# Kernel optimization log

Measured on AMD Instinct MI355X. Metric: run time of the kernel, lower is better.

Reference implementation:

```python
import jax, jax.numpy as jnp
import numpy as np
from jax import lax

N = 2048
D_ENC = 64      # conv channels
D = 512         # node embedding dim (resnet18 feature dim)
K = 5           # max_num_neighbors
L_LAYERS = 4    # num_layers
ARENA = 32.0    # positions scaled to [0, ARENA)^2
R2 = 2.0        # radius^2 = (sqrt(2))^2


def setup_inputs() -> dict:
    key = jax.random.key(0)
    ks = jax.random.split(key, 9)
    imgs = jax.random.normal(ks[0], (N, 3, 64, 64), dtype=jnp.float32)
    pos = jax.random.uniform(ks[1], (N, 2), dtype=jnp.float32)  # scaled by ARENA inside
    conv_w = jax.random.normal(ks[2], (D_ENC, 3, 7, 7), dtype=jnp.float32) * 0.05
    conv_b = jnp.zeros((D_ENC,), dtype=jnp.float32)
    proj_w = jax.random.normal(ks[3], (D_ENC, D), dtype=jnp.float32) * (1.0 / np.sqrt(D_ENC))
    proj_b = jnp.zeros((D,), dtype=jnp.float32)
    w_self = jax.random.normal(ks[4], (L_LAYERS, D, D), dtype=jnp.float32) * (1.0 / np.sqrt(D))
    w_nbr = jax.random.normal(ks[5], (L_LAYERS, D, D), dtype=jnp.float32) * (1.0 / np.sqrt(D))
    b_gnn = jnp.zeros((L_LAYERS, D), dtype=jnp.float32)
    return {"imgs": imgs, "pos": pos, "conv_w": conv_w, "conv_b": conv_b,
            "proj_w": proj_w, "proj_b": proj_b,
            "w_self": w_self, "w_nbr": w_nbr, "b_gnn": b_gnn}


def _encode(imgs, conv_w, conv_b, proj_w, proj_b):
    # conv 7x7 stride 2 + relu + global avg pool + linear -> [N, D]
    x = lax.conv_general_dilated(imgs, conv_w, window_strides=(2, 2), padding="SAME",
                                 dimension_numbers=("NCHW", "OIHW", "NCHW"))
    x = jax.nn.relu(x + conv_b[None, :, None, None])
    x = x.mean(axis=(2, 3))                      # [N, D_ENC]
    return jax.nn.relu(x @ proj_w + proj_b)      # [N, D]


def _radius_knn(pos):
    # radius graph with radius sqrt(2), no self loops, capped at K neighbors
    p = pos * ARENA                              # [N, 2]
    d2 = jnp.sum((p[:, None, :] - p[None, :, :]) ** 2, axis=-1)  # [N, N]
    invalid = (d2 > R2) | jnp.eye(N, dtype=bool)
    d2m = jnp.where(invalid, jnp.inf, d2)
    neg_vals, idx = lax.top_k(-d2m, K)           # K nearest within radius
    valid = jnp.isfinite(neg_vals)               # [N, K]
    return idx, valid


def reference(imgs, pos, conv_w, conv_b, proj_w, proj_b, w_self, w_nbr, b_gnn):
    h = _encode(imgs, conv_w, conv_b, proj_w, proj_b)   # [N, D]
    idx, valid = _radius_knn(pos)                        # [N, K], [N, K]
    vmask = valid.astype(h.dtype)                        # [N, K]
    denom = jnp.maximum(vmask.sum(axis=1, keepdims=True), 1.0)  # [N, 1]
    for l in range(L_LAYERS):
        nbr = h[idx] * vmask[:, :, None]                 # [N, K, D] gather
        agg = nbr.sum(axis=1) / denom                    # mean over valid neighbors
        h = jax.nn.relu(h @ w_self[l] + agg @ w_nbr[l] + b_gnn[l])
    return h
```

## Files before the change

### kernel.cpp

```cpp
#include <hip/hip_runtime.h>


#define NNODES 2048

typedef __attribute__((ext_vector_type(8))) _Float16 half8;
typedef __attribute__((ext_vector_type(16))) float f32x16;

__device__ inline uint pack2h(float x, float y) {
  ushort a = __builtin_bit_cast(ushort, (_Float16)x);
  ushort b = __builtin_bit_cast(ushort, (_Float16)y);
  return (uint)a | ((uint)b << 16);
}

__global__ __launch_bounds__(256) void setup_kernel(
    const float* __restrict__ conv_w, const float* __restrict__ wsrc_s,
    const float* __restrict__ wsrc_n, const float* __restrict__ pos,
    ushort* __restrict__ wfrag, ushort* __restrict__ wT,
    int* __restrict__ nbr, float* __restrict__ den, float* __restrict__ enc) {
  __shared__ float4 smem4[1040];
  const int bid = blockIdx.x;
  const int tid = threadIdx.x;

  if (bid < 44) {
    int i = bid * 256 + tid;
    int j = i & 7;
    int l = (i >> 3) & 63;
    int q = i >> 9;
    int kb = q % 11, ct = q / 11;
    int g = 2 * kb + (l >> 5);
    int c = 32 * ct + (l & 31);
    float val = 0.f;
    if (g < 21 && j < 7) val = conv_w[c * 147 + g * 7 + j];
    wfrag[i] = __builtin_bit_cast(ushort, (_Float16)val);
    return;
  }

  if (bid < 556) {
    float(*s)[65] = (float(*)[65])smem4;
    int bid2 = bid - 44;
    int m = bid2 >> 6, kt = (bid2 >> 3) & 7, nt = bid2 & 7;
    const float* in = (m < 4) ? (wsrc_s + m * 262144) : (wsrc_n + (m - 4) * 262144);
    ushort* out = wT + m * 262144;
    int k0 = kt << 6, n0 = nt << 6;
#pragma unroll
    for (int rep = 0; rep < 4; ++rep) {
      int row = (rep << 4) + (tid >> 4);
      int c4 = (tid & 15) << 2;
      float4 v = *(const float4*)&in[(k0 + row) * 512 + n0 + c4];
      s[row][c4] = v.x; s[row][c4 + 1] = v.y; s[row][c4 + 2] = v.z; s[row][c4 + 3] = v.w;
    }
    __syncthreads();
#pragma unroll
    for (int rep = 0; rep < 4; ++rep) {
      int n = (rep << 4) + (tid >> 4);
      int k4 = (tid & 15) << 2;
      ushort4 o;
      o.x = __builtin_bit_cast(ushort, (_Float16)s[k4 + 0][n]);
      o.y = __builtin_bit_cast(ushort, (_Float16)s[k4 + 1][n]);
      o.z = __builtin_bit_cast(ushort, (_Float16)s[k4 + 2][n]);
      o.w = __builtin_bit_cast(ushort, (_Float16)s[k4 + 3][n]);
      *(ushort4*)&out[(n0 + n) * 512 + k0 + k4] = o;
    }
    return;
  }

  {
    float* s_d2 = (float*)smem4;
    int* s_idx = (int*)(s_d2 + NNODES);
    int* s_cnt = (int*)(s_idx + NNODES);
    const int i = bid - 556;
    if (tid < 16) {
      float4 z4 = {0.f, 0.f, 0.f, 0.f};
      ((float4*)(enc + i * 64))[tid] = z4;
    }
    if (tid == 0) *s_cnt = 0;
    __syncthreads();
    const float px = pos[2 * i] * 32.f, py = pos[2 * i + 1] * 32.f;
#pragma unroll
    for (int r = 0; r < 8; ++r) {
      int j = tid + (r << 8);
      float2 q = ((const float2*)pos)[j];
      float dx = q.x * 32.f - px, dy = q.y * 32.f - py;
      float d2 = dx * dx + dy * dy;
      if (d2 <= 2.0f && j != i) {
        int slot = atomicAdd(s_cnt, 1);
        s_d2[slot] = d2;
        s_idx[slot] = j;
      }
    }
    __syncthreads();
    if (tid < 64) {
      const int lane = tid;
      const int cnt = *s_cnt;
      int nf = 0;
#pragma unroll
      for (int k = 0; k < 5; ++k) {
        float best = 1e30f;
        int bslot = 0x7fffffff;
        for (int e = lane; e < cnt; e += 64) {
          float d = s_d2[e];
          if (d < best) { best = d; bslot = e; }
        }
#pragma unroll
        for (int off = 1; off < 64; off <<= 1) {
          float od = __shfl_xor(best, off);
          int os = __shfl_xor(bslot, off);
          if (od < best || (od == best && os < bslot)) { best = od; bslot = os; }
        }
        bool got = (best < 1e30f);
        if (lane == 0) nbr[i * 5 + k] = got ? s_idx[bslot] : -1;
        if (got) { s_d2[bslot] = 1e30f; ++nf; }
      }
      if (lane == 0) den[i] = 1.f / (float)(nf > 0 ? nf : 1);
    }
  }
}

__global__ __launch_bounds__(256) void conv_pool_kernel(
    const float* __restrict__ imgs, const ushort* __restrict__ wfrag,
    const float* __restrict__ cb, float* __restrict__ enc) {
  __shared__ int4 s_all[2471];
  ushort* s_img = (ushort*)s_all;
  const half8* swf8 = (const half8*)((char*)s_all + 15984);
  float* s_pool = (float*)((char*)s_all + 38512);

  const int n = blockIdx.x >> 1;
  const int r0half = blockIdx.x & 1;
  const int wy = 32 * r0half - 2;
  const int tid = threadIdx.x;
  const int lane = tid & 63;
  const int w = tid >> 6;
  const int hi = lane >> 5;
  const int lo = lane & 31;

  int4 z = {0, 0, 0, 0};
  for (int i = tid; i < 999; i += 256) s_all[i] = z;
  __syncthreads();

  {
    const int4* wf4 = (const int4*)wfrag;
    int4* swf4 = (int4*)((char*)s_all + 15984);
    for (int i = tid; i < 1408; i += 256) swf4[i] = wf4[i];
  }

  const float4* src = (const float4*)(imgs + (size_t)n * 12288);
  for (int i = tid; i < 1776; i += 256) {
    int ic = i / 592;
    int rem = i - ic * 592;
    int li = rem >> 4, xq = rem & 15;
    int iy = wy + li;
    if (iy >= 0 && iy < 64) {
      float4 v = src[(ic * 64 + iy) * 16 + xq];
      int d = (ic * 37 + li) * 72 + (xq << 2) + 2;
      ((uint*)s_img)[d >> 1] = pack2h(v.x, v.y);
      ((uint*)s_img)[(d >> 1) + 1] = pack2h(v.z, v.w);
    }
  }

  int aoff[11];
#pragma unroll
  for (int kb = 0; kb < 11; ++kb) {
    int g = 2 * kb + hi;
    if (g > 20) g = 20;
    int ic = g / 7, ky = g - ic * 7;
    aoff[kb] = (ic * 37 + ky) * 144 + 4 * lo + w * 1152;
  }
  const float bias0 = cb[lo];
  const float bias1 = cb[32 + lo];
  __syncthreads();

  const char* sb = (const char*)s_img;
  union F { half8 v; uint u[4]; };
  F A0, A1, A2, A3, C0, C1, C2, C3;
  half8 B0, B1, D0, D1;
  f32x16 acc00 = {}, acc01 = {}, acc10 = {}, acc11 = {};
  f32x16 acc20 = {}, acc21 = {}, acc30 = {}, acc31 = {};

#define LOADSET(AA0, AA1, AA2, AA3, BB0, BB1, KB) do {                        \
    const char* p_ = (const char*)__builtin_assume_aligned(sb + aoff[KB], 4); \
    __builtin_memcpy(&AA0.u[0], p_,        8);                                \
    __builtin_memcpy(&AA0.u[2], p_ + 8,    8);                                \
    __builtin_memcpy(&AA1.u[0], p_ + 288,  8);                                \
    __builtin_memcpy(&AA1.u[2], p_ + 296,  8);                                \
    __builtin_memcpy(&AA2.u[0], p_ + 576,  8);                                \
    __builtin_memcpy(&AA2.u[2], p_ + 584,  8);                                \
    __builtin_memcpy(&AA3.u[0], p_ + 864,  8);                                \
    __builtin_memcpy(&AA3.u[2], p_ + 872,  8);                                \
    BB0 = swf8[(KB) * 64 + lane];                                             \
    BB1 = swf8[(11 + (KB)) * 64 + lane];                                      \
  } while (0)

#define MFMA8(AA0, AA1, AA2, AA3, BB0, BB1) do {                              \
    __builtin_amdgcn_s_setprio(1);                                            \
    acc00 = __builtin_amdgcn_mfma_f32_32x32x16_f16(AA0.v, BB0, acc00, 0, 0, 0); \
    acc01 = __builtin_amdgcn_mfma_f32_32x32x16_f16(AA0.v, BB1, acc01, 0, 0, 0); \
    acc10 = __builtin_amdgcn_mfma_f32_32x32x16_f16(AA1.v, BB0, acc10, 0, 0, 0); \
    acc11 = __builtin_amdgcn_mfma_f32_32x32x16_f16(AA1.v, BB1, acc11, 0, 0, 0); \
    acc20 = __builtin_amdgcn_mfma_f32_32x32x16_f16(AA2.v, BB0, acc20, 0, 0, 0); \
    acc21 = __builtin_amdgcn_mfma_f32_32x32x16_f16(AA2.v, BB1, acc21, 0, 0, 0); \
    acc30 = __builtin_amdgcn_mfma_f32_32x32x16_f16(AA3.v, BB0, acc30, 0, 0, 0); \
    acc31 = __builtin_amdgcn_mfma_f32_32x32x16_f16(AA3.v, BB1, acc31, 0, 0, 0); \
    __builtin_amdgcn_s_setprio(0);                                            \
  } while (0)

  LOADSET(A0, A1, A2, A3, B0, B1, 0);
#pragma unroll
  for (int kb = 0; kb < 10; kb += 2) {
    LOADSET(C0, C1, C2, C3, D0, D1, kb + 1);
    MFMA8(A0, A1, A2, A3, B0, B1);
    LOADSET(A0, A1, A2, A3, B0, B1, kb + 2);
    MFMA8(C0, C1, C2, C3, D0, D1);
  }
  MFMA8(A0, A1, A2, A3, B0, B1);
#undef LOADSET
#undef MFMA8

  float s0 = 0.f, s1 = 0.f;
#pragma unroll
  for (int r = 0; r < 16; ++r) {
    s0 += fmaxf(acc00[r] + bias0, 0.f) + fmaxf(acc10[r] + bias0, 0.f)
        + fmaxf(acc20[r] + bias0, 0.f) + fmaxf(acc30[r] + bias0, 0.f);
    s1 += fmaxf(acc01[r] + bias1, 0.f) + fmaxf(acc11[r] + bias1, 0.f)
        + fmaxf(acc21[r] + bias1, 0.f) + fmaxf(acc31[r] + bias1, 0.f);
  }
  s0 += __shfl_xor(s0, 32);
  s1 += __shfl_xor(s1, 32);
  if (lane < 32) {
    s_pool[w * 64 + lo] = s0;
    s_pool[w * 64 + 32 + lo] = s1;
  }
  __syncthreads();
  if (tid < 64) {
    float s = s_pool[tid] + s_pool[64 + tid] + s_pool[128 + tid] + s_pool[192 + tid];
    atomicAdd(&enc[n * 64 + tid], s * (1.f / 1024.f));
  }
}

__global__ __launch_bounds__(256) void proj_kernel(
    const float* __restrict__ enc, const float* __restrict__ pw,
    const float* __restrict__ pb, ushort* __restrict__ h16) {
  int c = ((blockIdx.x & 1) << 8) | threadIdx.x;
  int r0 = (blockIdx.x >> 1) << 3;
  float bias = pb[c];
  float acc[8];
#pragma unroll
  for (int r = 0; r < 8; ++r) acc[r] = bias;
#pragma unroll 4
  for (int k = 0; k < 64; ++k) {
    float w = pw[k * 512 + c];
#pragma unroll
    for (int r = 0; r < 8; ++r) acc[r] = fmaf(enc[(r0 + r) * 64 + k], w, acc[r]);
  }
#pragma unroll
  for (int r = 0; r < 8; ++r)
    h16[(r0 + r) * 512 + c] = __builtin_bit_cast(ushort, (_Float16)fmaxf(acc[r], 0.f));
}

__global__ __launch_bounds__(256) void gnn_gemm_kernel(
    const ushort* __restrict__ h16, const int* __restrict__ nbr,
    const float* __restrict__ den,
    const ushort* __restrict__ Ws, const ushort* __restrict__ Wn,
    const float* __restrict__ bias, ushort* __restrict__ hout,
    float* __restrict__ fout, int final_layer) {
  __shared__ ushort s_lds[2][16384];
  __shared__ int s_nbr[320];
  __shared__ float s_den[64];
  const int tid = threadIdx.x;
  const int lane = tid & 63;
  const int hi = lane >> 5, lo = lane & 31;
  const int wu = __builtin_amdgcn_readfirstlane(tid >> 6);
  const int wr = wu >> 1, wc = wu & 1;
  const int bm = blockIdx.x >> 3, bn = blockIdx.x & 7;
  const int r0 = bm << 6, c0 = bn << 6;

  if (tid < 80) ((int4*)s_nbr)[tid] = ((const int4*)(nbr + r0 * 5))[tid];
  else if (tid < 96) ((float4*)s_den)[tid - 80] = ((const float4*)(den + r0))[tid - 80];
  __syncthreads();

  const int grow = tid >> 2, gseg = tid & 3;
  int gj[5];
  uint gm[5];
#pragma unroll
  for (int k = 0; k < 5; ++k) {
    int j = s_nbr[grow * 5 + k];
    gm[k] = (j >= 0) ? 0xFFFFFFFFu : 0u;
    gj[k] = (j >= 0) ? j : 0;
  }
  half8 den8;
  {
    _Float16 dh = (_Float16)s_den[grow];
#pragma unroll
    for (int e = 0; e < 8; ++e) den8[e] = dh;
  }

  union GU { half8 v; uint u[4]; };
  GU ga[5][2];

  auto GATHER = [&](int it) {
    const ushort* hb = h16 + (it << 6) + gseg * 16;
#pragma unroll
    for (int k = 0; k < 5; ++k) {
      const half8* p = (const half8*)(hb + gj[k] * 512);
      ga[k][0].v = p[0];
      ga[k][1].v = p[1];
    }
  };
  auto COMBINE = [&](int buf) {
#pragma unroll
    for (int part = 0; part < 2; ++part) {
      GU t0, t1, t2, t3, t4;
#pragma unroll
      for (int j2 = 0; j2 < 4; ++j2) {
        t0.u[j2] = ga[0][part].u[j2] & gm[0];
        t1.u[j2] = ga[1][part].u[j2] & gm[1];
        t2.u[j2] = ga[2][part].u[j2] & gm[2];
        t3.u[j2] = ga[3][part].u[j2] & gm[3];
        t4.u[j2] = ga[4][part].u[j2] & gm[4];
      }
      half8 s = ((t0.v + t1.v) + (t2.v + t3.v)) + t4.v;
      s = s * den8;
      *(half8*)&s_lds[buf][4096 + (2 * gseg + part) * 512 + grow * 8] = s;
    }
  };
  auto STAGE = [&](int buf, int it) {
    int k0 = it << 6;
    const ushort* ph = h16 + (r0 + lane) * 512 + k0 + 8 * wu;
    const ushort* ps = Ws + (c0 + lane) * 512 + k0 + 8 * wu;
    const ushort* pn = Wn + (c0 + lane) * 512 + k0 + 8 * wu;
    ushort* lb = &s_lds[buf][wu << 9];
#define GLDS(SRC, DST) __builtin_amdgcn_global_load_lds( \
      (const __attribute__((address_space(1))) void*)(SRC), \
      (__attribute__((address_space(3))) void*)(DST), 16, 0, 0)
    GLDS(ph, lb);            GLDS(ph + 32, lb + 2048);
    GLDS(ps, lb + 8192);     GLDS(ps + 32, lb + 10240);
    GLDS(pn, lb + 12288);    GLDS(pn + 32, lb + 14336);
#undef GLDS
  };

  f32x16 accS = {}, accN = {};
  GATHER(0);
  STAGE(0, 0);
  COMBINE(0);
  __syncthreads();
  int cur = 0;
  for (int it = 0; it < 8; ++it) {
    if (it < 7) {
      GATHER(it + 1);
      STAGE(cur ^ 1, it + 1);
    }
    const half8* pAh = (const half8*)&s_lds[cur][0];
    const half8* pAg = (const half8*)&s_lds[cur][4096];
    const half8* pBs = (const half8*)&s_lds[cur][8192];
    const half8* pBn = (const half8*)&s_lds[cur][12288];
#pragma unroll
    for (int ks = 0; ks < 4; ++ks) {
      int gi = (2 * ks + hi) * 64;
      half8 ah = pAh[gi + 32 * wr + lo];
      half8 bs = pBs[gi + 32 * wc + lo];
      accS = __builtin_amdgcn_mfma_f32_32x32x16_f16(ah, bs, accS, 0, 0, 0);
      half8 ag = pAg[gi + 32 * wr + lo];
      half8 bn2 = pBn[gi + 32 * wc + lo];
      accN = __builtin_amdgcn_mfma_f32_32x32x16_f16(ag, bn2, accN, 0, 0, 0);
    }
    if (it < 7) COMBINE(cur ^ 1);
    __syncthreads();
    cur ^= 1;
  }

  const int col = c0 + 32 * wc + lo;
  const float b = bias[col];
#pragma unroll
  for (int r = 0; r < 16; ++r) {
    int row = r0 + 32 * wr + (r & 3) + ((r >> 2) << 3) + (hi << 2);
    float v = fmaxf(accS[r] + accN[r] + b, 0.f);
    if (final_layer) fout[row * 512 + col] = v;
    else hout[row * 512 + col] = __builtin_bit_cast(ushort, (_Float16)v);
  }
}

extern "C" void kernel_launch(void* const* d_in, const int* in_sizes, int n_in,
                              void* d_out, int out_size, void* d_ws, size_t ws_size,
                              hipStream_t stream) {
  const float* imgs   = (const float*)d_in[0];
  const float* pos    = (const float*)d_in[1];
  const float* conv_w = (const float*)d_in[2];
  const float* conv_b = (const float*)d_in[3];
  const float* proj_w = (const float*)d_in[4];
  const float* proj_b = (const float*)d_in[5];
  const float* w_self = (const float*)d_in[6];
  const float* w_nbr  = (const float*)d_in[7];
  const float* b_gnn  = (const float*)d_in[8];

  char* ws = (char*)d_ws;
  ushort* wfrag = (ushort*)(ws);
  float*  enc   = (float*) (ws + 32768);
  ushort* h16a  = (ushort*)(ws + 557056);
  ushort* h16b  = (ushort*)(ws + 2654208);
  ushort* wT16  = (ushort*)(ws + 6848512);
  int*    nbr   = (int*)   (ws + 11042816);
  float*  den   = (float*) (ws + 11083776);

  setup_kernel<<<2604, 256, 0, stream>>>(conv_w, w_self, w_nbr, pos,
                                         wfrag, wT16, nbr, den, enc);
  conv_pool_kernel<<<2 * NNODES, 256, 0, stream>>>(imgs, wfrag, conv_b, enc);
  proj_kernel<<<512, 256, 0, stream>>>(enc, proj_w, proj_b, h16a);

  for (int l = 0; l < 4; ++l) {
    ushort* hin  = (l & 1) ? h16b : h16a;
    ushort* hnew = (l & 1) ? h16a : h16b;
    gnn_gemm_kernel<<<256, 256, 0, stream>>>(
        hin, nbr, den, wT16 + l * 262144, wT16 + (4 + l) * 262144,
        b_gnn + l * 512, hnew, (float*)d_out, (l == 3) ? 1 : 0);
  }
}
```

Baseline: 158.3 us.

## Split conv MFMA into two row passes, async-load weights to LDS, raise occupancy

Restructures the conv MFMA loop to process the four row tiles in two passes of two, halving the live accumulator registers, and sets launch bounds to request four blocks per CU. Weight fragments are now copied to LDS with global_load_lds direct-to-LDS instructions issued before the first barrier, overlapping with the LDS zeroing and avoiding the register round-trip. A-operand addressing uses precomputed bases with constant offsets instead of an offset array. The trade-off is that B fragments are reloaded from LDS in each pass, and the larger unrolled code may add instruction overhead.

```diff
diff --git a/kernel.cpp b/kernel.cpp
--- a/kernel.cpp
+++ b/kernel.cpp
@@ -116,12 +116,11 @@
   }
 }
 
-__global__ __launch_bounds__(256) void conv_pool_kernel(
+__global__ __launch_bounds__(256, 4) void conv_pool_kernel(
     const float* __restrict__ imgs, const ushort* __restrict__ wfrag,
     const float* __restrict__ cb, float* __restrict__ enc) {
   __shared__ int4 s_all[2471];
   ushort* s_img = (ushort*)s_all;
-  const half8* swf8 = (const half8*)((char*)s_all + 15984);
   float* s_pool = (float*)((char*)s_all + 38512);
 
   const int n = blockIdx.x >> 1;
@@ -135,13 +134,22 @@
 
   int4 z = {0, 0, 0, 0};
   for (int i = tid; i < 999; i += 256) s_all[i] = z;
+
+  {
+    char* ldsb = (char*)s_all + 15984;
+#pragma unroll
+    for (int r = 0; r < 5; ++r) {
+      __builtin_amdgcn_global_load_lds(
+          (const __attribute__((address_space(1))) void*)(wfrag + (r * 256 + tid) * 8),
+          (__attribute__((address_space(3))) void*)(ldsb + (r * 256 + tid) * 16), 16, 0, 0);
+    }
+    if (tid < 128) {
+      __builtin_amdgcn_global_load_lds(
+          (const __attribute__((address_space(1))) void*)(wfrag + (1280 + tid) * 8),
+          (__attribute__((address_space(3))) void*)(ldsb + (1280 + tid) * 16), 16, 0, 0);
+    }
+  }
   __syncthreads();
-
-  {
-    const int4* wf4 = (const int4*)wfrag;
-    int4* swf4 = (int4*)((char*)s_all + 15984);
-    for (int i = tid; i < 1408; i += 256) swf4[i] = wf4[i];
-  }
 
   const float4* src = (const float4*)(imgs + (size_t)n * 12288);
   for (int i = tid; i < 1776; i += 256) {
@@ -157,77 +165,84 @@
     }
   }
 
-  int aoff[11];
-#pragma unroll
-  for (int kb = 0; kb < 11; ++kb) {
-    int g = 2 * kb + hi;
-    if (g > 20) g = 20;
-    int ic = g / 7, ky = g - ic * 7;
-    aoff[kb] = (ic * 37 + ky) * 144 + 4 * lo + w * 1152;
-  }
   const float bias0 = cb[lo];
   const float bias1 = cb[32 + lo];
   __syncthreads();
 
   const char* sb = (const char*)s_img;
+  const char* baseA = sb + 4 * lo + w * 1152 + (hi ? 144 : 0);
+  const char* baseA3 = sb + 4 * lo + w * 1152 + (hi ? 5328 : 864);
+  const char* baseB = (const char*)s_all + 15984 + lane * 16;
+
+
   union F { half8 v; uint u[4]; };
-  F A0, A1, A2, A3, C0, C1, C2, C3;
-  half8 B0, B1, D0, D1;
-  f32x16 acc00 = {}, acc01 = {}, acc10 = {}, acc11 = {};
-  f32x16 acc20 = {}, acc21 = {}, acc30 = {}, acc31 = {};
-
-#define LOADSET(AA0, AA1, AA2, AA3, BB0, BB1, KB) do {                        \
-    const char* p_ = (const char*)__builtin_assume_aligned(sb + aoff[KB], 4); \
-    __builtin_memcpy(&AA0.u[0], p_,        8);                                \
-    __builtin_memcpy(&AA0.u[2], p_ + 8,    8);                                \
-    __builtin_memcpy(&AA1.u[0], p_ + 288,  8);                                \
-    __builtin_memcpy(&AA1.u[2], p_ + 296,  8);                                \
-    __builtin_memcpy(&AA2.u[0], p_ + 576,  8);                                \
-    __builtin_memcpy(&AA2.u[2], p_ + 584,  8);                                \
-    __builtin_memcpy(&AA3.u[0], p_ + 864,  8);                                \
-    __builtin_memcpy(&AA3.u[2], p_ + 872,  8);                                \
-    BB0 = swf8[(KB) * 64 + lane];                                             \
-    BB1 = swf8[(11 + (KB)) * 64 + lane];                                      \
+  float poolacc0 = 0.f, poolacc1 = 0.f;
+
+#define LOADA(F0, F1, BASE, OFF, TP) do {                                     \
+    const uint* p_ = (const uint*)((BASE) + (OFF) + (TP) * 576);              \
+    F0.u[0] = p_[0]; F0.u[1] = p_[1]; F0.u[2] = p_[2]; F0.u[3] = p_[3];       \
+    const uint* q_ = (const uint*)((BASE) + (OFF) + (TP) * 576 + 288);        \
+    F1.u[0] = q_[0]; F1.u[1] = q_[1]; F1.u[2] = q_[2]; F1.u[3] = q_[3];       \
   } while (0)
-
-#define MFMA8(AA0, AA1, AA2, AA3, BB0, BB1) do {                              \
+#define LOADB(B0, B1, KB) do {                                                \
+    B0 = *(const half8*)(baseB + (KB) * 1024);                                \
+    B1 = *(const half8*)(baseB + 11264 + (KB) * 1024);                        \
+  } while (0)
+#define MFMA4(FF0, FF1, BB0, BB1) do {                                        \
     __builtin_amdgcn_s_setprio(1);                                            \
-    acc00 = __builtin_amdgcn_mfma_f32_32x32x16_f16(AA0.v, BB0, acc00, 0, 0, 0); \
-    acc01 = __builtin_amdgcn_mfma_f32_32x32x16_f16(AA0.v, BB1, acc01, 0, 0, 0); \
-    acc10 = __builtin_amdgcn_mfma_f32_32x32x16_f16(AA1.v, BB0, acc10, 0, 0, 0); \
-    acc11 = __builtin_amdgcn_mfma_f32_32x32x16_f16(AA1.v, BB1, acc11, 0, 0, 0); \
-    acc20 = __builtin_amdgcn_mfma_f32_32x32x16_f16(AA2.v, BB0, acc20, 0, 0, 0); \
-    acc21 = __builtin_amdgcn_mfma_f32_32x32x16_f16(AA2.v, BB1, acc21, 0, 0, 0); \
-    acc30 = __builtin_amdgcn_mfma_f32_32x32x16_f16(AA3.v, BB0, acc30, 0, 0, 0); \
-    acc31 = __builtin_amdgcn_mfma_f32_32x32x16_f16(AA3.v, BB1, acc31, 0, 0, 0); \
+    a0 = __builtin_amdgcn_mfma_f32_32x32x16_f16(FF0.v, BB0, a0, 0, 0, 0);     \
+    a1 = __builtin_amdgcn_mfma_f32_32x32x16_f16(FF0.v, BB1, a1, 0, 0, 0);     \
+    a2 = __builtin_amdgcn_mfma_f32_32x32x16_f16(FF1.v, BB0, a2, 0, 0, 0);     \
+    a3 = __builtin_amdgcn_mfma_f32_32x32x16_f16(FF1.v, BB1, a3, 0, 0, 0);     \
     __builtin_amdgcn_s_setprio(0);                                            \
   } while (0)
 
-  LOADSET(A0, A1, A2, A3, B0, B1, 0);
-#pragma unroll
-  for (int kb = 0; kb < 10; kb += 2) {
-    LOADSET(C0, C1, C2, C3, D0, D1, kb + 1);
-    MFMA8(A0, A1, A2, A3, B0, B1);
-    LOADSET(A0, A1, A2, A3, B0, B1, kb + 2);
-    MFMA8(C0, C1, C2, C3, D0, D1);
-  }
-  MFMA8(A0, A1, A2, A3, B0, B1);
-#undef LOADSET
-#undef MFMA8
-
-  float s0 = 0.f, s1 = 0.f;
-#pragma unroll
-  for (int r = 0; r < 16; ++r) {
-    s0 += fmaxf(acc00[r] + bias0, 0.f) + fmaxf(acc10[r] + bias0, 0.f)
-        + fmaxf(acc20[r] + bias0, 0.f) + fmaxf(acc30[r] + bias0, 0.f);
-    s1 += fmaxf(acc01[r] + bias1, 0.f) + fmaxf(acc11[r] + bias1, 0.f)
-        + fmaxf(acc21[r] + bias1, 0.f) + fmaxf(acc31[r] + bias1, 0.f);
-  }
-  s0 += __shfl_xor(s0, 32);
-  s1 += __shfl_xor(s1, 32);
+#pragma unroll
+  for (int tp = 0; tp < 2; ++tp) {
+    f32x16 a0 = {}, a1 = {}, a2 = {}, a3 = {};
+    F f0a, f1a, f0b, f1b;
+    half8 b0a, b1a, b0b, b1b;
+    LOADA(f0a, f1a, baseA, 0, tp);        LOADB(b0a, b1a, 0);
+    LOADA(f0b, f1b, baseA, 288, tp);      LOADB(b0b, b1b, 1);
+    MFMA4(f0a, f1a, b0a, b1a);
+    LOADA(f0a, f1a, baseA, 576, tp);      LOADB(b0a, b1a, 2);
+    MFMA4(f0b, f1b, b0b, b1b);
+    LOADA(f0b, f1b, baseA3, 0, tp);       LOADB(b0b, b1b, 3);
+    MFMA4(f0a, f1a, b0a, b1a);
+    LOADA(f0a, f1a, baseA, 5472, tp);     LOADB(b0a, b1a, 4);
+    MFMA4(f0b, f1b, b0b, b1b);
+    LOADA(f0b, f1b, baseA, 5760, tp);     LOADB(b0b, b1b, 5);
+    MFMA4(f0a, f1a, b0a, b1a);
+    LOADA(f0a, f1a, baseA, 6048, tp);     LOADB(b0a, b1a, 6);
+    MFMA4(f0b, f1b, b0b, b1b);
+    LOADA(f0b, f1b, baseA, 10656, tp);    LOADB(b0b, b1b, 7);
+    MFMA4(f0a, f1a, b0a, b1a);
+    LOADA(f0a, f1a, baseA, 10944, tp);    LOADB(b0a, b1a, 8);
+    MFMA4(f0b, f1b, b0b, b1b);
+    LOADA(f0b, f1b, baseA, 11232, tp);    LOADB(b0b, b1b, 9);
+    MFMA4(f0a, f1a, b0a, b1a);
+    LOADA(f0a, f1a, baseA, 11520, tp);    LOADB(b0a, b1a, 10);
+    MFMA4(f0b, f1b, b0b, b1b);
+    MFMA4(f0a, f1a, b0a, b1a);
+
+    float s0 = 0.f, s1 = 0.f;
+#pragma unroll
+    for (int r = 0; r < 16; ++r) {
+      s0 += fmaxf(a0[r] + bias0, 0.f) + fmaxf(a2[r] + bias0, 0.f);
+      s1 += fmaxf(a1[r] + bias1, 0.f) + fmaxf(a3[r] + bias1, 0.f);
+    }
+    poolacc0 += s0;
+    poolacc1 += s1;
+  }
+#undef LOADA
+#undef LOADB
+#undef MFMA4
+
+  poolacc0 += __shfl_xor(poolacc0, 32);
+  poolacc1 += __shfl_xor(poolacc1, 32);
   if (lane < 32) {
-    s_pool[w * 64 + lo] = s0;
-    s_pool[w * 64 + 32 + lo] = s1;
+    s_pool[w * 64 + lo] = poolacc0;
+    s_pool[w * 64 + 32 + lo] = poolacc1;
   }
   __syncthreads();
   if (tid < 64) {
```

Result: slower. 218.9 us (+38.2%).
